# Performance work log

Hardware: AMD Instinct MI355X
Metric: run time of the kernel (lower is better)

Reference implementation:

```python
import jax, jax.numpy as jnp
import numpy as np

F_IN = 128
HID = 256
OUT = 64
E = 500_000
NP_ALL = 304_096   # paper nodes: seed 4096 + hop1 100000 + hop2 200000
NP_H01 = 104_096   # paper nodes kept at layer 1 (seed + hop1)
NA_ALL = 154_096   # author nodes: 4096 + 50000 + 100000
NA_H01 = 54_096    # author nodes kept at layer 1


def setup_inputs() -> dict:
    key = jax.random.key(0)
    ks = iter(jax.random.split(key, 40))
    def nrm(shape, scale=0.05):
        return jax.random.normal(next(ks), shape, dtype=jnp.float32) * scale
    inp = {
        'x_paper': nrm((NP_ALL, F_IN), 1.0),
        'x_author': nrm((NA_ALL, F_IN), 1.0),
    }
    # per-layer, per-edge-type SAGEConv params: lin_l (W,b on aggregated msgs), lin_r (W, no bias, on dst)
    for li, fin in ((0, F_IN), (1, HID)):
        for rel in ('cites', 'writes', 'rev'):
            inp[f'l{li}_{rel}_Wl'] = nrm((fin, HID))
            inp[f'l{li}_{rel}_b'] = jnp.zeros((HID,), jnp.float32)
            inp[f'l{li}_{rel}_Wr'] = nrm((fin, HID))
    inp['lin_W'] = nrm((HID, OUT))
    inp['lin_b'] = jnp.zeros((OUT,), jnp.float32)
    # edge_index per edge type per sampled hop; hop-1 edges survive trimming at layer 1
    for name, hi in (('e_cites_h1', NP_H01), ('e_cites_h2', NP_ALL),
                     ('e_writes_h1', NA_H01), ('e_writes_h2', NA_ALL),
                     ('e_rev_h1', NA_H01), ('e_rev_h2', NA_ALL)):
        inp[name] = jax.random.randint(next(ks), (2, E), 0, hi, dtype=jnp.int32)
    return inp


def _sage(x_src, x_dst, edge, Wl, b, Wr):
    # SAGEConv: mean-aggregate neighbor features, lin_l(agg) + b + lin_r(x_dst)
    n_dst = x_dst.shape[0]
    msg = x_src[edge[0]]  # [E, F] gather
    s = jax.ops.segment_sum(msg, edge[1], num_segments=n_dst)
    cnt = jax.ops.segment_sum(jnp.ones((edge.shape[1],), x_src.dtype), edge[1], num_segments=n_dst)
    mean = s / jnp.maximum(cnt, 1.0)[:, None]  # 0 for isolated dst nodes (PyG mean)
    return mean @ Wl + b + x_dst @ Wr


def reference(x_paper, x_author,
              l0_cites_Wl, l0_cites_b, l0_cites_Wr,
              l0_writes_Wl, l0_writes_b, l0_writes_Wr,
              l0_rev_Wl, l0_rev_b, l0_rev_Wr,
              l1_cites_Wl, l1_cites_b, l1_cites_Wr,
              l1_writes_Wl, l1_writes_b, l1_writes_Wr,
              l1_rev_Wl, l1_rev_b, l1_rev_Wr,
              lin_W, lin_b,
              e_cites_h1, e_cites_h2, e_writes_h1, e_writes_h2, e_rev_h1, e_rev_h2):
    # ---- layer 0: no trimming -> all nodes, all (hop1+hop2) edges ----
    ec = jnp.concatenate([e_cites_h1, e_cites_h2], axis=1)
    ew = jnp.concatenate([e_writes_h1, e_writes_h2], axis=1)
    er = jnp.concatenate([e_rev_h1, e_rev_h2], axis=1)
    p = _sage(x_paper, x_paper, ec, l0_cites_Wl, l0_cites_b, l0_cites_Wr) \
      + _sage(x_author, x_paper, ew, l0_writes_Wl, l0_writes_b, l0_writes_Wr)
    a = _sage(x_paper, x_author, er, l0_rev_Wl, l0_rev_b, l0_rev_Wr)
    xp, xa = jax.nn.relu(p), jax.nn.relu(a)
    # ---- layer 1: trim_to_layer drops last hop nodes + hop-2 edges ----
    xp, xa = xp[:NP_H01], xa[:NA_H01]
    p = _sage(xp, xp, e_cites_h1, l1_cites_Wl, l1_cites_b, l1_cites_Wr) \
      + _sage(xa, xp, e_writes_h1, l1_writes_Wl, l1_writes_b, l1_writes_Wr)
    xp = jax.nn.relu(p)
    # final Linear on 'paper' features
    return xp @ lin_W + lin_b
```

## Files before the change

kernel.cpp:

```cpp
#include <hip/hip_runtime.h>

typedef unsigned short u16;
typedef unsigned int   u32;
typedef __bf16  bf16x8 __attribute__((ext_vector_type(8)));
typedef float   floatx4 __attribute__((ext_vector_type(4)));

#define NP_ALL 304096
#define NP_H01 104096
#define NA_ALL 154096
#define NA_H01 54096

#define SEG_C0 0
#define SEG_W0 104096
#define SEG_R0 208192
#define SEG_C1 262288
#define SEG_W1 366384
#define SCAN_N 470480
#define SCAN_NBLK 1838

__device__ __forceinline__ u16 f2bf(float f){
    u32 u = __float_as_uint(f);
    return (u16)((u + 0x7fffu + ((u>>16)&1u)) >> 16);
}
__device__ __forceinline__ float blo(u32 v){ return __uint_as_float(v<<16); }
__device__ __forceinline__ float bhi(u32 v){ return __uint_as_float(v & 0xFFFF0000u); }

__global__ void wcvt_k(u16* __restrict__ dst, const float* __restrict__ src, int n){
    int t = blockIdx.x*256 + threadIdx.x;
    if (t < n) dst[t] = f2bf(src[t]);
}
__global__ void wadd_k(u16* __restrict__ dst, const float* __restrict__ a, const float* __restrict__ b, int n){
    int t = blockIdx.x*256 + threadIdx.x;
    if (t < n) dst[t] = f2bf(a[t] + b[t]);
}
__global__ void bias_k(float* __restrict__ dst, const float* __restrict__ a, const float* __restrict__ b, int n){
    int t = blockIdx.x*256 + threadIdx.x;
    if (t < n) dst[t] = a[t] + (b ? b[t] : 0.0f);
}
__global__ void cvt2_k(u32* __restrict__ dst, const float* __restrict__ src, int n2){
    int t = blockIdx.x*256 + threadIdx.x;
    if (t >= n2) return;
    dst[t] = (u32)f2bf(src[2*t]) | ((u32)f2bf(src[2*t+1])<<16);
}
__global__ void repack_k(const u16* __restrict__ Wc, int K, int N, u16* __restrict__ Wp){
    int t = blockIdx.x*256 + threadIdx.x;
    int total = (K>>5)*(N>>4)*64;
    if (t >= total) return;
    int lane = t & 63;
    int nt = (t>>6) % (N>>4);
    int kt = (t>>6) / (N>>4);
    int n  = nt*16 + (lane & 15);
    int k0 = kt*32 + (lane>>4)*8;
    u16* dst = Wp + (size_t)t*8;
    #pragma unroll
    for (int j=0;j<8;j++) dst[j] = Wc[(size_t)(k0+j)*N + n];
}

__global__ void hist_k(const int* __restrict__ edst, int nE, int limit, int* __restrict__ deg){
    int t = blockIdx.x*256 + threadIdx.x;
    if (t >= nE) return;
    int d = edst[t];
    if (d < limit) atomicAdd(deg + d, 1);
}
__global__ void scan1_k(const int* __restrict__ deg, int* __restrict__ bsum){
    __shared__ int sm[256];
    int t = blockIdx.x*256 + threadIdx.x;
    sm[threadIdx.x] = (t < SCAN_N) ? deg[t] : 0;
    __syncthreads();
    for (int s=128; s>0; s>>=1){
        if (threadIdx.x < s) sm[threadIdx.x] += sm[threadIdx.x+s];
        __syncthreads();
    }
    if (threadIdx.x == 0) bsum[blockIdx.x] = sm[0];
}
__global__ void scan2_k(int* __restrict__ bsum, int n){
    __shared__ int sm[256];
    int chunk = (n + 255) >> 8;
    int st = threadIdx.x * chunk;
    int sum = 0;
    for (int i=0;i<chunk;i++){ int idx = st+i; if (idx < n) sum += bsum[idx]; }
    sm[threadIdx.x] = sum; __syncthreads();
    int acc = sum;
    for (int s=1; s<256; s<<=1){
        int t2 = (threadIdx.x >= s) ? sm[threadIdx.x - s] : 0;
        __syncthreads();
        acc += t2; sm[threadIdx.x] = acc;
        __syncthreads();
    }
    int excl = acc - sum;
    for (int i=0;i<chunk;i++){
        int idx = st+i;
        if (idx < n){ int v = bsum[idx]; bsum[idx] = excl; excl += v; }
    }
}
__global__ void scan3_k(const int* __restrict__ deg, const int* __restrict__ bsum,
                        int* __restrict__ rowptr, int* __restrict__ wp){
    __shared__ int sm[256];
    int t = blockIdx.x*256 + threadIdx.x;
    int v = (t < SCAN_N) ? deg[t] : 0;
    sm[threadIdx.x] = v; __syncthreads();
    int acc = v;
    for (int s=1; s<256; s<<=1){
        int t2 = (threadIdx.x >= s) ? sm[threadIdx.x - s] : 0;
        __syncthreads();
        acc += t2; sm[threadIdx.x] = acc;
        __syncthreads();
    }
    int excl = acc - v + bsum[blockIdx.x];
    if (t < SCAN_N){ rowptr[t] = excl; wp[t] = excl; }
    if (t == SCAN_N-1) rowptr[SCAN_N] = excl + v;
}
__global__ void fill_k(const int* __restrict__ esrc, const int* __restrict__ edst,
                       int nE, int limit, int* __restrict__ wp, int* __restrict__ pool){
    int t = blockIdx.x*256 + threadIdx.x;
    if (t >= nE) return;
    int d = edst[t];
    if (d >= limit) return;
    int p = atomicAdd(wp + d, 1);
    pool[p] = esrc[t];
}

template<int D>
__device__ __forceinline__ void gather_mean(
    const u16* __restrict__ src, int ld,
    const int* __restrict__ rowptr, int seg, int d,
    const int* __restrict__ pool, int lane, u16* __restrict__ outrow)
{
    int b = rowptr[seg + d], e = rowptr[seg + d + 1];
    float rc = 1.0f / (float)((e - b) > 1 ? (e - b) : 1);
    if (D == 128) {
        float a0=0,a1=0,c0=0,c1=0;
        int i = b;
        for (; i+1 < e; i += 2){
            int s0 = pool[i], s1 = pool[i+1];
            u32 v0 = *(const u32*)(src + (size_t)s0*ld + 2*lane);
            u32 v1 = *(const u32*)(src + (size_t)s1*ld + 2*lane);
            a0 += blo(v0); a1 += bhi(v0);
            c0 += blo(v1); c1 += bhi(v1);
        }
        if (i < e){
            int s0 = pool[i];
            u32 v0 = *(const u32*)(src + (size_t)s0*ld + 2*lane);
            a0 += blo(v0); a1 += bhi(v0);
        }
        u32 lo = f2bf((a0+c0)*rc), hi = f2bf((a1+c1)*rc);
        *(u32*)(outrow + 2*lane) = lo | (hi<<16);
    } else {
        float a0=0,a1=0,a2=0,a3=0,c0=0,c1=0,c2=0,c3=0;
        int i = b;
        for (; i+1 < e; i += 2){
            int s0 = pool[i], s1 = pool[i+1];
            uint2 v0 = *(const uint2*)(src + (size_t)s0*ld + 4*lane);
            uint2 v1 = *(const uint2*)(src + (size_t)s1*ld + 4*lane);
            a0 += blo(v0.x); a1 += bhi(v0.x); a2 += blo(v0.y); a3 += bhi(v0.y);
            c0 += blo(v1.x); c1 += bhi(v1.x); c2 += blo(v1.y); c3 += bhi(v1.y);
        }
        if (i < e){
            int s0 = pool[i];
            uint2 v0 = *(const uint2*)(src + (size_t)s0*ld + 4*lane);
            a0 += blo(v0.x); a1 += bhi(v0.x); a2 += blo(v0.y); a3 += bhi(v0.y);
        }
        uint2 o;
        o.x = (u32)f2bf((a0+c0)*rc) | ((u32)f2bf((a1+c1)*rc)<<16);
        o.y = (u32)f2bf((a2+c2)*rc) | ((u32)f2bf((a3+c3)*rc)<<16);
        *(uint2*)(outrow + 4*lane) = o;
    }
}

__global__ __launch_bounds__(256) void gAp_k(
    const u16* __restrict__ xpb, const u16* __restrict__ xab,
    const int* __restrict__ rowptr, const int* __restrict__ pool,
    u16* __restrict__ Ap)
{
    int gid = blockIdx.x*256 + threadIdx.x;
    int wid = gid >> 6, lane = gid & 63;
    if (wid >= NP_H01) return;
    u16* row = Ap + (size_t)wid*384;
    gather_mean<128>(xpb, 128, rowptr, SEG_C0, wid, pool, lane, row);
    gather_mean<128>(xab, 128, rowptr, SEG_W0, wid, pool, lane, row + 128);
    *(u32*)(row + 256 + 2*lane) = *(const u32*)(xpb + (size_t)wid*128 + 2*lane);
}
__global__ __launch_bounds__(256) void gAa_k(
    const u16* __restrict__ xpb, const u16* __restrict__ xab,
    const int* __restrict__ rowptr, const int* __restrict__ pool,
    u16* __restrict__ Aa)
{
    int gid = blockIdx.x*256 + threadIdx.x;
    int wid = gid >> 6, lane = gid & 63;
    if (wid >= NA_H01) return;
    u16* row = Aa + (size_t)wid*256;
    gather_mean<128>(xpb, 128, rowptr, SEG_R0, wid, pool, lane, row);
    *(u32*)(row + 128 + 2*lane) = *(const u32*)(xab + (size_t)wid*128 + 2*lane);
}
__global__ __launch_bounds__(256) void gA1_k(
    const u16* __restrict__ xp, const u16* __restrict__ xa,
    const int* __restrict__ rowptr, const int* __restrict__ pool,
    u16* __restrict__ A1)
{
    int gid = blockIdx.x*256 + threadIdx.x;
    int wid = gid >> 6, lane = gid & 63;
    if (wid >= NP_H01) return;
    u16* row = A1 + (size_t)wid*768;
    gather_mean<256>(xp, 768, rowptr, SEG_C1, wid, pool, lane, row);
    gather_mean<256>(xa, 256, rowptr, SEG_W1, wid, pool, lane, row + 256);
}

template<int WROWS, int WCOLS, int WMT, int WNT, bool RELU, bool F32OUT>
__global__ __launch_bounds__(256, 2) void gemm3_k(
    const u16* __restrict__ A, int lda, int M, int K,
    const u16* __restrict__ Wp, int nt16, const float* __restrict__ bias,
    void* __restrict__ C_, int ldc)
{
    constexpr int BNT  = WCOLS*WNT;
    constexpr int BM   = WROWS*WMT*16;
    constexpr int NSTG = 2*BNT;
    constexpr int PERW = NSTG/4;
    static_assert(2*WMT == 8, "vmcnt(8) literal assumes 8 A-loads per stage");
    __shared__ __align__(16) u16 ldsB[2*NSTG*512];

    int wave = threadIdx.x >> 6, lane = threadIdx.x & 63;
    int quad = lane >> 4, l15 = lane & 15;
    int wr = wave / WCOLS, wc = wave % WCOLS;
    int bm0 = blockIdx.x * BM;
    int ntb = blockIdx.y * BNT;

    floatx4 acc[WMT][WNT];
    #pragma unroll
    for (int i=0;i<WMT;i++)
        #pragma unroll
        for (int j=0;j<WNT;j++) acc[i][j] = (floatx4){0.f,0.f,0.f,0.f};

    const u16* Abase[WMT];
    #pragma unroll
    for (int i=0;i<WMT;i++){
        int r = bm0 + (wr*WMT + i)*16 + l15;
        r = (r < M) ? r : (M-1);
        Abase[i] = A + (size_t)r*lda + quad*8;
    }

    int nstages = K >> 6;

    auto stage_issue = [&](int sn, int bufsel){
        #pragma unroll
        for (int i=0;i<PERW;i++){
            int g = wave*PERW + i;
            int ktl = g / BNT, ntl = g % BNT;
            const u16* gp = Wp + ((size_t)(sn*2+ktl)*nt16 + ntb + ntl)*512 + lane*8;
            u16* lp = ldsB + bufsel*(NSTG*512) + g*512 + lane*8;
            __builtin_amdgcn_global_load_lds(
                (const __attribute__((address_space(1))) void*)gp,
                (__attribute__((address_space(3))) void*)lp, 16, 0, 0);
        }
    };
    auto a_issue = [&](int sn, bf16x8 (&dst)[2][WMT]){
        #pragma unroll
        for (int ktl=0; ktl<2; ktl++)
            #pragma unroll
            for (int i=0;i<WMT;i++)
                dst[ktl][i] = *(const bf16x8*)(Abase[i] + (size_t)sn*64 + ktl*32);
    };
    auto compute = [&](int bufsel, bf16x8 (&af)[2][WMT]){
        const u16* lb = ldsB + bufsel*(NSTG*512);
        #pragma unroll
        for (int ktl=0; ktl<2; ktl++){
            bf16x8 bfr[WNT];
            #pragma unroll
            for (int j=0;j<WNT;j++)
                bfr[j] = *(const bf16x8*)(lb + ((size_t)(ktl*BNT + wc*WNT + j)*64 + lane)*8);
            #pragma unroll
            for (int i=0;i<WMT;i++)
                #pragma unroll
                for (int j=0;j<WNT;j++)
                    acc[i][j] = __builtin_amdgcn_mfma_f32_16x16x32_bf16(af[ktl][i], bfr[j], acc[i][j], 0,0,0);
        }
    };

    bf16x8 aA[2][WMT], aB[2][WMT];
    stage_issue(0, 0);
    __builtin_amdgcn_sched_barrier(0);
    a_issue(0, aA);
    __builtin_amdgcn_sched_barrier(0);

    for (int s=0; s<nstages; s+=2){
        asm volatile("s_waitcnt lgkmcnt(0)" ::: "memory");
        asm volatile("s_waitcnt vmcnt(8)"  ::: "memory");
        __builtin_amdgcn_sched_barrier(0);
        __builtin_amdgcn_s_barrier();
        {
            int sn = s+1;
            stage_issue(sn, 1);
            __builtin_amdgcn_sched_barrier(0);
            a_issue(sn, aB);
            __builtin_amdgcn_sched_barrier(0);
            compute(0, aA);
        }
        asm volatile("s_waitcnt lgkmcnt(0)" ::: "memory");
        asm volatile("s_waitcnt vmcnt(8)"  ::: "memory");
        __builtin_amdgcn_sched_barrier(0);
        __builtin_amdgcn_s_barrier();
        {
            int sn = (s+2 < nstages) ? s+2 : 0;
            stage_issue(sn, 0);
            __builtin_amdgcn_sched_barrier(0);
            a_issue(sn, aA);
            __builtin_amdgcn_sched_barrier(0);
            compute(1, aB);
        }
    }
    asm volatile("s_waitcnt vmcnt(0)" ::: "memory");

    #pragma unroll
    for (int j=0;j<WNT;j++){
        int col = (ntb + wc*WNT + j)*16 + l15;
        float bv = bias[col];
        #pragma unroll
        for (int i=0;i<WMT;i++){
            int rbase = bm0 + (wr*WMT + i)*16 + quad*4;
            #pragma unroll
            for (int ii=0; ii<4; ii++){
                int row = rbase + ii;
                if (row < M){
                    float v = acc[i][j][ii] + bv;
                    if (RELU) v = fmaxf(v, 0.0f);
                    if (F32OUT) ((float*)C_)[(size_t)row*ldc + col] = v;
                    else        ((u16*)C_)[(size_t)row*ldc + col] = f2bf(v);
                }
            }
        }
    }
}

extern "C" void kernel_launch(void* const* d_in, const int* in_sizes, int n_in,
                              void* d_out, int out_size, void* d_ws, size_t ws_size,
                              hipStream_t stream)
{
    const float* x_paper  = (const float*)d_in[0];
    const float* x_author = (const float*)d_in[1];
    const float* w_in[22];
    for (int i=0;i<22;i++) w_in[i] = (const float*)d_in[i];
    const int* e_c1 = (const int*)d_in[22]; int nE_c1 = in_sizes[22]/2;
    const int* e_c2 = (const int*)d_in[23]; int nE_c2 = in_sizes[23]/2;
    const int* e_w1 = (const int*)d_in[24]; int nE_w1 = in_sizes[24]/2;
    const int* e_w2 = (const int*)d_in[25]; int nE_w2 = in_sizes[25]/2;
    const int* e_r1 = (const int*)d_in[26]; int nE_r1 = in_sizes[26]/2;
    const int* e_r2 = (const int*)d_in[27]; int nE_r2 = in_sizes[27]/2;
    float* out = (float*)d_out;

    size_t off = 0;
    auto take = [&](size_t nb)->void* {
        void* p = (char*)d_ws + off;
        off = (off + nb + 255) & ~(size_t)255;
        return p;
    };
    u16*   A1  = (u16*)take((size_t)NP_H01*768*2);
    u16*   xa  = (u16*)take((size_t)NA_H01*256*2);
    u16*   Ap  = (u16*)take((size_t)NP_H01*384*2);
    u16*   Aa  = (u16*)take((size_t)NA_H01*256*2);
    int*   deg    = (int*)take((size_t)SCAN_N*4);
    int*   rowptr = (int*)take((size_t)(SCAN_N+1)*4);
    int*   wp     = (int*)take((size_t)SCAN_N*4);
    int*   bsum   = (int*)take((size_t)SCAN_NBLK*4);
    int*   pool   = (int*)take((size_t)4000000*4);
    u16* Wc0p = (u16*)take((size_t)384*256*2);
    u16* Wc0a = (u16*)take((size_t)256*256*2);
    u16* Wc1  = (u16*)take((size_t)768*256*2);
    u16* Wcf  = (u16*)take((size_t)256*64*2);
    u16* Wp0p = (u16*)take((size_t)384*256*2);
    u16* Wp0a = (u16*)take((size_t)256*256*2);
    u16* Wp1  = (u16*)take((size_t)768*256*2);
    u16* Wpf  = (u16*)take((size_t)256*64*2);
    float* b0p = (float*)take(256*4);
    float* b0a = (float*)take(256*4);
    float* b1  = (float*)take(256*4);
    float* bfin= (float*)take(64*4);

    u16* xpb = A1;
    u16* xab = A1 + (size_t)NP_ALL*128;
    u16* h1  = Ap;

    auto cdiv = [](long a, long b){ return (int)((a + b - 1)/b); };
    dim3 B(256);

    hipMemsetAsync(deg, 0, (size_t)SCAN_N*4, stream);

    wcvt_k<<<cdiv(32768,256),B,0,stream>>>(Wc0p,        w_in[2], 32768);
    wcvt_k<<<cdiv(32768,256),B,0,stream>>>(Wc0p+32768,  w_in[5], 32768);
    wadd_k<<<cdiv(32768,256),B,0,stream>>>(Wc0p+65536,  w_in[4], w_in[7], 32768);
    wcvt_k<<<cdiv(32768,256),B,0,stream>>>(Wc0a,        w_in[8], 32768);
    wcvt_k<<<cdiv(32768,256),B,0,stream>>>(Wc0a+32768,  w_in[10], 32768);
    wcvt_k<<<cdiv(65536,256),B,0,stream>>>(Wc1,         w_in[11], 65536);
    wcvt_k<<<cdiv(65536,256),B,0,stream>>>(Wc1+65536,   w_in[14], 65536);
    wadd_k<<<cdiv(65536,256),B,0,stream>>>(Wc1+131072,  w_in[13], w_in[16], 65536);
    wcvt_k<<<cdiv(16384,256),B,0,stream>>>(Wcf,         w_in[20], 16384);
    bias_k<<<1,B,0,stream>>>(b0p, w_in[3],  w_in[6],  256);
    bias_k<<<1,B,0,stream>>>(b0a, w_in[9],  nullptr,  256);
    bias_k<<<1,B,0,stream>>>(b1,  w_in[12], w_in[15], 256);
    bias_k<<<1,B,0,stream>>>(bfin,w_in[21], nullptr,  64);
    repack_k<<<cdiv(12288,256),B,0,stream>>>(Wc0p, 384, 256, Wp0p);
    repack_k<<<cdiv( 8192,256),B,0,stream>>>(Wc0a, 256, 256, Wp0a);
    repack_k<<<cdiv(24576,256),B,0,stream>>>(Wc1,  768, 256, Wp1);
    repack_k<<<cdiv( 2048,256),B,0,stream>>>(Wcf,  256,  64, Wpf);
    int n2p = NP_ALL*128/2, n2a = NA_ALL*128/2;
    cvt2_k<<<cdiv(n2p,256),B,0,stream>>>((u32*)xpb, x_paper,  n2p);
    cvt2_k<<<cdiv(n2a,256),B,0,stream>>>((u32*)xab, x_author, n2a);

    hist_k<<<cdiv(nE_c1,256),B,0,stream>>>(e_c1+nE_c1, nE_c1, NP_H01, deg+SEG_C0);
    hist_k<<<cdiv(nE_c2,256),B,0,stream>>>(e_c2+nE_c2, nE_c2, NP_H01, deg+SEG_C0);
    hist_k<<<cdiv(nE_w1,256),B,0,stream>>>(e_w1+nE_w1, nE_w1, NP_H01, deg+SEG_W0);
    hist_k<<<cdiv(nE_w2,256),B,0,stream>>>(e_w2+nE_w2, nE_w2, NP_H01, deg+SEG_W0);
    hist_k<<<cdiv(nE_r1,256),B,0,stream>>>(e_r1+nE_r1, nE_r1, NA_H01, deg+SEG_R0);
    hist_k<<<cdiv(nE_r2,256),B,0,stream>>>(e_r2+nE_r2, nE_r2, NA_H01, deg+SEG_R0);
    hist_k<<<cdiv(nE_c1,256),B,0,stream>>>(e_c1+nE_c1, nE_c1, NP_H01, deg+SEG_C1);
    hist_k<<<cdiv(nE_w1,256),B,0,stream>>>(e_w1+nE_w1, nE_w1, NP_H01, deg+SEG_W1);
    scan1_k<<<SCAN_NBLK,B,0,stream>>>(deg, bsum);
    scan2_k<<<1,B,0,stream>>>(bsum, SCAN_NBLK);
    scan3_k<<<SCAN_NBLK,B,0,stream>>>(deg, bsum, rowptr, wp);
    fill_k<<<cdiv(nE_c1,256),B,0,stream>>>(e_c1, e_c1+nE_c1, nE_c1, NP_H01, wp+SEG_C0, pool);
    fill_k<<<cdiv(nE_c2,256),B,0,stream>>>(e_c2, e_c2+nE_c2, nE_c2, NP_H01, wp+SEG_C0, pool);
    fill_k<<<cdiv(nE_w1,256),B,0,stream>>>(e_w1, e_w1+nE_w1, nE_w1, NP_H01, wp+SEG_W0, pool);
    fill_k<<<cdiv(nE_w2,256),B,0,stream>>>(e_w2, e_w2+nE_w2, nE_w2, NP_H01, wp+SEG_W0, pool);
    fill_k<<<cdiv(nE_r1,256),B,0,stream>>>(e_r1, e_r1+nE_r1, nE_r1, NA_H01, wp+SEG_R0, pool);
    fill_k<<<cdiv(nE_r2,256),B,0,stream>>>(e_r2, e_r2+nE_r2, nE_r2, NA_H01, wp+SEG_R0, pool);
    fill_k<<<cdiv(nE_c1,256),B,0,stream>>>(e_c1, e_c1+nE_c1, nE_c1, NP_H01, wp+SEG_C1, pool);
    fill_k<<<cdiv(nE_w1,256),B,0,stream>>>(e_w1, e_w1+nE_w1, nE_w1, NP_H01, wp+SEG_W1, pool);

    gAp_k<<<cdiv((long)NP_H01*64,256),B,0,stream>>>(xpb, xab, rowptr, pool, Ap);
    gAa_k<<<cdiv((long)NA_H01*64,256),B,0,stream>>>(xpb, xab, rowptr, pool, Aa);

    {
        dim3 g(cdiv(NP_H01,128), 2);
        gemm3_k<2,2,4,4,true,false><<<g,B,0,stream>>>(Ap, 384, NP_H01, 384, Wp0p, 16, b0p, A1+512, 768);
    }
    {
        dim3 g(cdiv(NA_H01,128), 2);
        gemm3_k<2,2,4,4,true,false><<<g,B,0,stream>>>(Aa, 256, NA_H01, 256, Wp0a, 16, b0a, xa, 256);
    }

    gA1_k<<<cdiv((long)NP_H01*64,256),B,0,stream>>>(A1+512, xa, rowptr, pool, A1);

    {
        dim3 g(cdiv(NP_H01,128), 2);
        gemm3_k<2,2,4,4,true,false><<<g,B,0,stream>>>(A1, 768, NP_H01, 768, Wp1, 16, b1, h1, 256);
    }
    {
        dim3 g(cdiv(NP_H01,256), 1);
        gemm3_k<4,1,4,4,false,true><<<g,B,0,stream>>>(h1, 256, NP_H01, 256, Wpf, 4, bfin, out, 64);
    }
}
```

Baseline: 1.266 ms.

## Store GEMM A operands in K-tiled 64-column panel layout

Reorganizes the gathered activation matrices (Ap, Aa, A1, h1) into K-panels of 64 columns stored contiguously per row, so each GEMM stage reads a dense M×64 slab instead of strided rows. The gather kernels write into the panel layout and the GEMM epilogue can emit panel-tiled output for the next stage. The intent is better cache-line and TLB locality for the A-operand loads. The cost is more complex indexing, and the gA1 reads of the layer-0 output now stride within panels.

```diff
diff --git a/kernel.cpp b/kernel.cpp
--- a/kernel.cpp
+++ b/kernel.cpp
@@ -122,9 +122,9 @@
 
 template<int D>
 __device__ __forceinline__ void gather_mean(
-    const u16* __restrict__ src, int ld,
+    const u16* __restrict__ srcl, size_t rstride,
     const int* __restrict__ rowptr, int seg, int d,
-    const int* __restrict__ pool, int lane, u16* __restrict__ outrow)
+    const int* __restrict__ pool, u16* __restrict__ outl)
 {
     int b = rowptr[seg + d], e = rowptr[seg + d + 1];
     float rc = 1.0f / (float)((e - b) > 1 ? (e - b) : 1);
@@ -133,39 +133,40 @@
         int i = b;
         for (; i+1 < e; i += 2){
             int s0 = pool[i], s1 = pool[i+1];
-            u32 v0 = *(const u32*)(src + (size_t)s0*ld + 2*lane);
-            u32 v1 = *(const u32*)(src + (size_t)s1*ld + 2*lane);
+            u32 v0 = *(const u32*)(srcl + (size_t)s0*rstride);
+            u32 v1 = *(const u32*)(srcl + (size_t)s1*rstride);
             a0 += blo(v0); a1 += bhi(v0);
             c0 += blo(v1); c1 += bhi(v1);
         }
         if (i < e){
             int s0 = pool[i];
-            u32 v0 = *(const u32*)(src + (size_t)s0*ld + 2*lane);
+            u32 v0 = *(const u32*)(srcl + (size_t)s0*rstride);
             a0 += blo(v0); a1 += bhi(v0);
         }
         u32 lo = f2bf((a0+c0)*rc), hi = f2bf((a1+c1)*rc);
-        *(u32*)(outrow + 2*lane) = lo | (hi<<16);
+        *(u32*)outl = lo | (hi<<16);
     } else {
         float a0=0,a1=0,a2=0,a3=0,c0=0,c1=0,c2=0,c3=0;
         int i = b;
         for (; i+1 < e; i += 2){
             int s0 = pool[i], s1 = pool[i+1];
-            uint2 v0 = *(const uint2*)(src + (size_t)s0*ld + 4*lane);
-            uint2 v1 = *(const uint2*)(src + (size_t)s1*ld + 4*lane);
+            uint2 v0 = *(const uint2*)(srcl + (size_t)s0*rstride);
+            uint2 v1 = *(const uint2*)(srcl + (size_t)s1*rstride);
             a0 += blo(v0.x); a1 += bhi(v0.x); a2 += blo(v0.y); a3 += bhi(v0.y);
             c0 += blo(v1.x); c1 += bhi(v1.x); c2 += blo(v1.y); c3 += bhi(v1.y);
         }
         if (i < e){
             int s0 = pool[i];
-            uint2 v0 = *(const uint2*)(src + (size_t)s0*ld + 4*lane);
+            uint2 v0 = *(const uint2*)(srcl + (size_t)s0*rstride);
             a0 += blo(v0.x); a1 += bhi(v0.x); a2 += blo(v0.y); a3 += bhi(v0.y);
         }
         uint2 o;
         o.x = (u32)f2bf((a0+c0)*rc) | ((u32)f2bf((a1+c1)*rc)<<16);
         o.y = (u32)f2bf((a2+c2)*rc) | ((u32)f2bf((a3+c3)*rc)<<16);
-        *(uint2*)(outrow + 4*lane) = o;
-    }
-}
+        *(uint2*)outl = o;
+    }
+}
+
 
 __global__ __launch_bounds__(256) void gAp_k(
     const u16* __restrict__ xpb, const u16* __restrict__ xab,
@@ -175,10 +176,13 @@
     int gid = blockIdx.x*256 + threadIdx.x;
     int wid = gid >> 6, lane = gid & 63;
     if (wid >= NP_H01) return;
-    u16* row = Ap + (size_t)wid*384;
-    gather_mean<128>(xpb, 128, rowptr, SEG_C0, wid, pool, lane, row);
-    gather_mean<128>(xab, 128, rowptr, SEG_W0, wid, pool, lane, row + 128);
-    *(u32*)(row + 256 + 2*lane) = *(const u32*)(xpb + (size_t)wid*128 + 2*lane);
+    const size_t SM = (size_t)NP_H01*64;
+    size_t wofs = (size_t)wid*64 + 2*(lane&31);
+    int hs = lane>>5;
+    gather_mean<128>(xpb + 2*lane, 128, rowptr, SEG_C0, wid, pool, Ap + (size_t)(0+hs)*SM + wofs);
+    gather_mean<128>(xab + 2*lane, 128, rowptr, SEG_W0, wid, pool, Ap + (size_t)(2+hs)*SM + wofs);
+    u32 v = *(const u32*)(xpb + (size_t)wid*128 + 2*lane);
+    *(u32*)(Ap + (size_t)(4+hs)*SM + wofs) = v;
 }
 __global__ __launch_bounds__(256) void gAa_k(
     const u16* __restrict__ xpb, const u16* __restrict__ xab,
@@ -188,28 +192,36 @@
     int gid = blockIdx.x*256 + threadIdx.x;
     int wid = gid >> 6, lane = gid & 63;
     if (wid >= NA_H01) return;
-    u16* row = Aa + (size_t)wid*256;
-    gather_mean<128>(xpb, 128, rowptr, SEG_R0, wid, pool, lane, row);
-    *(u32*)(row + 128 + 2*lane) = *(const u32*)(xab + (size_t)wid*128 + 2*lane);
+    const size_t SM = (size_t)NA_H01*64;
+    size_t wofs = (size_t)wid*64 + 2*(lane&31);
+    int hs = lane>>5;
+    gather_mean<128>(xpb + 2*lane, 128, rowptr, SEG_R0, wid, pool, Aa + (size_t)(0+hs)*SM + wofs);
+    u32 v = *(const u32*)(xab + (size_t)wid*128 + 2*lane);
+    *(u32*)(Aa + (size_t)(2+hs)*SM + wofs) = v;
 }
 __global__ __launch_bounds__(256) void gA1_k(
-    const u16* __restrict__ xp, const u16* __restrict__ xa,
+    const u16* __restrict__ A1src,
+    const u16* __restrict__ xa,
     const int* __restrict__ rowptr, const int* __restrict__ pool,
     u16* __restrict__ A1)
 {
     int gid = blockIdx.x*256 + threadIdx.x;
     int wid = gid >> 6, lane = gid & 63;
     if (wid >= NP_H01) return;
-    u16* row = A1 + (size_t)wid*768;
-    gather_mean<256>(xp, 768, rowptr, SEG_C1, wid, pool, lane, row);
-    gather_mean<256>(xa, 256, rowptr, SEG_W1, wid, pool, lane, row + 256);
+    const size_t SM = (size_t)NP_H01*64;
+    int qs = lane>>4;
+    size_t wofs = (size_t)wid*64 + 4*(lane&15);
+    gather_mean<256>(A1src + (size_t)(8+qs)*SM + 4*(lane&15), 64,
+                     rowptr, SEG_C1, wid, pool, A1 + (size_t)(0+qs)*SM + wofs);
+    gather_mean<256>(xa + 4*lane, 256,
+                     rowptr, SEG_W1, wid, pool, A1 + (size_t)(4+qs)*SM + wofs);
 }
 
 template<int WROWS, int WCOLS, int WMT, int WNT, bool RELU, bool F32OUT>
-__global__ __launch_bounds__(256, 2) void gemm3_k(
-    const u16* __restrict__ A, int lda, int M, int K,
+__global__ __launch_bounds__(256, 2) void gemm4_k(
+    const u16* __restrict__ At, int M, int K,
     const u16* __restrict__ Wp, int nt16, const float* __restrict__ bias,
-    void* __restrict__ C_, int ldc)
+    void* __restrict__ C_, int ldc, int tileM, int colofs)
 {
     constexpr int BNT  = WCOLS*WNT;
     constexpr int BM   = WROWS*WMT*16;
@@ -223,6 +235,7 @@
     int wr = wave / WCOLS, wc = wave % WCOLS;
     int bm0 = blockIdx.x * BM;
     int ntb = blockIdx.y * BNT;
+    const size_t SMS = (size_t)M*64;
 
     floatx4 acc[WMT][WNT];
     #pragma unroll
@@ -235,7 +248,7 @@
     for (int i=0;i<WMT;i++){
         int r = bm0 + (wr*WMT + i)*16 + l15;
         r = (r < M) ? r : (M-1);
-        Abase[i] = A + (size_t)r*lda + quad*8;
+        Abase[i] = At + (size_t)r*64 + quad*8;
     }
 
     int nstages = K >> 6;
@@ -257,7 +270,7 @@
         for (int ktl=0; ktl<2; ktl++)
             #pragma unroll
             for (int i=0;i<WMT;i++)
-                dst[ktl][i] = *(const bf16x8*)(Abase[i] + (size_t)sn*64 + ktl*32);
+                dst[ktl][i] = *(const bf16x8*)(Abase[i] + (size_t)sn*SMS + ktl*32);
     };
     auto compute = [&](int bufsel, bf16x8 (&af)[2][WMT]){
         const u16* lb = ldsB + bufsel*(NSTG*512);
@@ -323,7 +336,12 @@
                     float v = acc[i][j][ii] + bv;
                     if (RELU) v = fmaxf(v, 0.0f);
                     if (F32OUT) ((float*)C_)[(size_t)row*ldc + col] = v;
-                    else        ((u16*)C_)[(size_t)row*ldc + col] = f2bf(v);
+                    else if (tileM > 0){
+                        int ct = col + colofs;
+                        ((u16*)C_)[((size_t)(ct>>6)*tileM + row)*64 + (ct&63)] = f2bf(v);
+                    } else {
+                        ((u16*)C_)[(size_t)row*ldc + col] = f2bf(v);
+                    }
                 }
             }
         }
@@ -429,21 +447,21 @@
 
     {
         dim3 g(cdiv(NP_H01,128), 2);
-        gemm3_k<2,2,4,4,true,false><<<g,B,0,stream>>>(Ap, 384, NP_H01, 384, Wp0p, 16, b0p, A1+512, 768);
+        gemm4_k<2,2,4,4,true,false><<<g,B,0,stream>>>(Ap, NP_H01, 384, Wp0p, 16, b0p, A1, 0, NP_H01, 512);
     }
     {
         dim3 g(cdiv(NA_H01,128), 2);
-        gemm3_k<2,2,4,4,true,false><<<g,B,0,stream>>>(Aa, 256, NA_H01, 256, Wp0a, 16, b0a, xa, 256);
-    }
-
-    gA1_k<<<cdiv((long)NP_H01*64,256),B,0,stream>>>(A1+512, xa, rowptr, pool, A1);
+        gemm4_k<2,2,4,4,true,false><<<g,B,0,stream>>>(Aa, NA_H01, 256, Wp0a, 16, b0a, xa, 256, 0, 0);
+    }
+
+    gA1_k<<<cdiv((long)NP_H01*64,256),B,0,stream>>>(A1, xa, rowptr, pool, A1);
 
     {
         dim3 g(cdiv(NP_H01,128), 2);
-        gemm3_k<2,2,4,4,true,false><<<g,B,0,stream>>>(A1, 768, NP_H01, 768, Wp1, 16, b1, h1, 256);
+        gemm4_k<2,2,4,4,true,false><<<g,B,0,stream>>>(A1, NP_H01, 768, Wp1, 16, b1, h1, 0, NP_H01, 0);
     }
     {
         dim3 g(cdiv(NP_H01,256), 1);
-        gemm3_k<4,1,4,4,false,true><<<g,B,0,stream>>>(h1, 256, NP_H01, 256, Wpf, 4, bfin, out, 64);
-    }
-}
+        gemm4_k<4,1,4,4,false,true><<<g,B,0,stream>>>(h1, NP_H01, 256, Wpf, 4, bfin, out, 64, 0, 0);
+    }
+}
```

Result: no change. 1.265 ms (-0.1%).
